# Kernel tuning notes

Measured on AMD Instinct MI355X. Metric: run time of the kernel, lower is better.

## Reference

```python
import jax, jax.numpy as jnp
import numpy as np
from jax import lax

N, D, K = 131072, 128, 1024
BETA = 1.0
EMA_DECAY = 0.85

def setup_inputs() -> dict:
    key = jax.random.key(0)
    k1, k2, k3, k4 = jax.random.split(key, 4)
    return {
        "x": jax.random.normal(k1, (N, D), dtype=jnp.float32),
        "embeddings": jax.random.uniform(k2, (D, K), dtype=jnp.float32),
        "ema_count": jax.random.uniform(k3, (K,), dtype=jnp.float32),
        "embeddings_sum": jax.random.uniform(k4, (D, K), dtype=jnp.float32),
    }

def reference(x, embeddings, ema_count, embeddings_sum):
    input_shape = x.shape
    flat = x.reshape(-1, D)                      # [N, D]
    # squared-euclidean distances via expanded ||a-b||^2
    sim = flat @ embeddings                      # [N, K]
    dist = (jnp.sum(flat ** 2, axis=1, keepdims=True)
            + jnp.sum(embeddings ** 2, axis=0)
            - 2.0 * sim)                         # [N, K]
    idx = jnp.argmin(dist, axis=1)               # [N] int
    # codebook lookup (gather instead of one-hot matmul)
    quantized = jnp.take(embeddings.T, idx, axis=0).reshape(input_shape)
    # EMA update (segment_sum instead of one-hot matmul scatter)
    count = jax.ops.segment_sum(jnp.ones((flat.shape[0],), flat.dtype), idx,
                                num_segments=K)                  # [K]
    ema_count_new = (1.0 - EMA_DECAY) * ema_count + EMA_DECAY * count
    sums = jax.ops.segment_sum(flat, idx, num_segments=K).T      # [D, K]
    embeddings_sum_new = (1.0 - EMA_DECAY) * embeddings_sum + EMA_DECAY * sums
    embeddings_new = embeddings_sum_new / jnp.maximum(ema_count_new, 1e-5)
    # losses (commitment added via add_loss in original)
    commitment_loss = jnp.mean((lax.stop_gradient(quantized) - x) ** 2)
    # straight-through estimator
    q_st = x + lax.stop_gradient(quantized - x)
    return q_st, embeddings_new, ema_count_new, embeddings_sum_new, BETA * commitment_loss
```

## Files before the change

kernel.cpp:

```cpp
#include <hip/hip_runtime.h>
#include <cfloat>
#include <cstdint>

#define NROWS 131072
#define DIMD  128
#define KCODE 1024
#define MARGIN 0.045f
#define RCAP  65536

typedef __attribute__((ext_vector_type(8))) _Float16 half8;
typedef __attribute__((ext_vector_type(4))) float f32x4;

union U4H8 { uint4 u; half8 h; };

#define WS_REFINE_CNT 0
#define WS_LOSS       8
#define WS_COUNTS     16
#define WS_SUMS       4608
#define WS_LPART      528896
#define WS_CURSOR     532992
#define WS_E2         537088
#define WS_ZERO_BYTES 541184
#define WS_ET         541184
#define WS_BHI        1065472
#define WS_BEST       1327616
#define WS_IDX        1589760
#define WS_ROWLIST    2114048
#define WS_REFINE     2638336
#define WS_PARTIALS   3162624

#define OUT_QST  ((size_t)0)
#define OUT_EMB  ((size_t)NROWS * DIMD)
#define OUT_CNT  (OUT_EMB + (size_t)DIMD * KCODE)
#define OUT_ES   (OUT_CNT + KCODE)
#define OUT_LOSS (OUT_ES + (size_t)DIMD * KCODE)

__device__ __forceinline__ unsigned f16pair(float a, float b) {
    union { _Float16 h[2]; unsigned u; } p;
    p.h[0] = (_Float16)a;
    p.h[1] = (_Float16)b;
    return p.u;
}

__global__ void vq_prep(const float* __restrict__ E, uint4* __restrict__ Bh,
                        float* __restrict__ ET, float* __restrict__ e2) {
    int gid = blockIdx.x * 256 + threadIdx.x;
    int l = gid & 63;
    int t = (gid >> 6) & 3;
    int NB = gid >> 8;
    int n = NB * 16 + (l & 15);
    int k0 = t * 32 + (l >> 4) * 8;
    float v[8];
    float ss = 0.f;
    #pragma unroll
    for (int j = 0; j < 8; ++j) {
        v[j] = E[(size_t)(k0 + j) * KCODE + n];
        ss = fmaf(v[j], v[j], ss);
    }
    Bh[gid] = make_uint4(f16pair(v[0], v[1]), f16pair(v[2], v[3]),
                         f16pair(v[4], v[5]), f16pair(v[6], v[7]));
    float4* et4 = (float4*)(ET + (size_t)n * DIMD + k0);
    et4[0] = make_float4(v[0], v[1], v[2], v[3]);
    et4[1] = make_float4(v[4], v[5], v[6], v[7]);
    atomicAdd(&e2[n], ss);
}


#define LOADB(bARR, ev_, nb_)                                     \
  { _Pragma("unroll")                                             \
    for (int t_ = 0; t_ < 4; ++t_)                                \
      bARR[t_] = Bh[((nb_) * 4 + t_) * 64 + l];                   \
    ev_ = e2[(nb_) * 16 + m]; }

#define COMPUTE_NB(nb_, bARR, ev_)                                           \
  {                                                                          \
    f32x4 acc[2];                                                            \
    _Pragma("unroll")                                                        \
    for (int mt_ = 0; mt_ < 2; ++mt_) acc[mt_] = (f32x4){0.f,0.f,0.f,0.f};   \
    _Pragma("unroll")                                                        \
    for (int t_ = 0; t_ < 4; ++t_) {                                         \
      U4H8 bh_; bh_.u = bARR[t_];                                            \
      _Pragma("unroll")                                                      \
      for (int mt_ = 0; mt_ < 2; ++mt_)                                      \
        acc[mt_] = __builtin_amdgcn_mfma_f32_16x16x32_f16(ah[mt_][t_], bh_.h,\
                                                          acc[mt_], 0, 0, 0);\
    }                                                                        \
    int col_ = (nb_) * 16 + m;                                               \
    _Pragma("unroll")                                                        \
    for (int mt_ = 0; mt_ < 2; ++mt_)                                        \
      _Pragma("unroll")                                                      \
      for (int r_ = 0; r_ < 4; ++r_) {                                       \
        float s_ = fmaf(-2.0f, acc[mt_][r_], ev_);                           \
        if (s_ < m1[mt_][r_]) {                                              \
          m2[mt_][r_] = m1[mt_][r_]; i2[mt_][r_] = i1[mt_][r_];              \
          m1[mt_][r_] = s_;          i1[mt_][r_] = col_;                     \
        } else if (s_ < m2[mt_][r_]) {                                       \
          m2[mt_][r_] = s_;          i2[mt_][r_] = col_;                     \
        }                                                                    \
      }                                                                      \
  }

__global__ __launch_bounds__(256, 2) void vq_argmin_mfma(
        const float* __restrict__ x, const uint4* __restrict__ Bh,
        const float* __restrict__ e2,
        int* __restrict__ idx, int* __restrict__ counts,
        int* __restrict__ refine_pairs, int* __restrict__ refine_cnt) {

    __shared__ int hist[KCODE];

    const int tid = threadIdx.x;
    const int w = tid >> 6, l = tid & 63;
    const int m = l & 15, q = l >> 4;
    const int rw = blockIdx.x * 128 + w * 32;

    uint4 bA[4], bB[4];
    float evA, evB;
    LOADB(bA, evA, 0);
    LOADB(bB, evB, 1);

    const float4* x4 = (const float4*)x;
    half8 ah[2][4];
    #pragma unroll
    for (int mt = 0; mt < 2; ++mt) {
        int row = rw + mt * 16 + m;
        #pragma unroll
        for (int t = 0; t < 4; ++t) {
            int c4 = t * 8 + q * 2;
            float4 va = x4[(size_t)row * 32 + c4];
            float4 vb = x4[(size_t)row * 32 + c4 + 1];
            half8 hh;
            hh[0] = (_Float16)va.x; hh[1] = (_Float16)va.y;
            hh[2] = (_Float16)va.z; hh[3] = (_Float16)va.w;
            hh[4] = (_Float16)vb.x; hh[5] = (_Float16)vb.y;
            hh[6] = (_Float16)vb.z; hh[7] = (_Float16)vb.w;
            ah[mt][t] = hh;
        }
    }

    float m1[2][4], m2[2][4];
    int i1[2][4], i2[2][4];
    #pragma unroll
    for (int a = 0; a < 2; ++a)
        #pragma unroll
        for (int r = 0; r < 4; ++r) {
            m1[a][r] = FLT_MAX; m2[a][r] = FLT_MAX;
            i1[a][r] = 0; i2[a][r] = 0;
        }

    for (int nb = 0; nb < 64; nb += 2) {
        COMPUTE_NB(nb, bA, evA);
        { int p = (nb + 2 <= 63) ? nb + 2 : 62; LOADB(bA, evA, p); }
        COMPUTE_NB(nb + 1, bB, evB);
        { int p = (nb + 3 <= 63) ? nb + 3 : 63; LOADB(bB, evB, p); }
    }

    #pragma unroll
    for (int mt = 0; mt < 2; ++mt)
        #pragma unroll
        for (int r = 0; r < 4; ++r) {
            float a1 = m1[mt][r], a2 = m2[mt][r];
            int ai1 = i1[mt][r], ai2 = i2[mt][r];
            #pragma unroll
            for (int off = 1; off < 16; off <<= 1) {
                float o1 = __shfl_xor(a1, off, 64);
                float o2 = __shfl_xor(a2, off, 64);
                int oi1 = __shfl_xor(ai1, off, 64);
                int oi2 = __shfl_xor(ai2, off, 64);
                bool take = (o1 < a1) || (o1 == a1 && oi1 < ai1);
                float w1 = take ? o1 : a1;  int wi1 = take ? oi1 : ai1;
                float l1 = take ? a1 : o1;  int li1 = take ? ai1 : oi1;
                float c2 = a2; int ci2 = ai2;
                if (o2 < c2 || (o2 == c2 && oi2 < ci2)) { c2 = o2; ci2 = oi2; }
                if (l1 < c2 || (l1 == c2 && li1 < ci2)) { c2 = l1; ci2 = li1; }
                a1 = w1; ai1 = wi1; a2 = c2; ai2 = ci2;
            }
            m1[mt][r] = a1; m2[mt][r] = a2;
            i1[mt][r] = ai1; i2[mt][r] = ai2;
        }

    for (int i = tid; i < KCODE; i += 256) hist[i] = 0;
    __syncthreads();
    if (m == 0) {
        #pragma unroll
        for (int mt = 0; mt < 2; ++mt)
            #pragma unroll
            for (int r = 0; r < 4; ++r) {
                int row = rw + mt * 16 + q * 4 + r;
                int bi = i1[mt][r];
                idx[row] = bi;
                atomicAdd(&hist[bi], 1);
                if (!(m2[mt][r] - m1[mt][r] > MARGIN)) {
                    int pos = atomicAdd(refine_cnt, 1);
                    if (pos < RCAP) {
                        refine_pairs[2 * pos]     = row;
                        refine_pairs[2 * pos + 1] = i2[mt][r];
                    }
                }
            }
    }
    __syncthreads();
    for (int i = tid; i < KCODE; i += 256) {
        int h = hist[i];
        if (h) atomicAdd(&counts[i], h);
    }
}

__global__ __launch_bounds__(256) void vq_refine2(
        const float* __restrict__ x, const float* __restrict__ ET,
        const float* __restrict__ e2,
        const int* __restrict__ refine_pairs, const int* __restrict__ refine_cnt,
        int* __restrict__ idx, int* __restrict__ counts) {
    int cnt = *refine_cnt;
    if (cnt > RCAP) cnt = RCAP;
    for (int e = blockIdx.x * 256 + threadIdx.x; e < cnt; e += gridDim.x * 256) {
        int n  = refine_pairs[2 * e];
        int kb = refine_pairs[2 * e + 1];
        int ka = idx[n];
        const float4* xa = (const float4*)(x + (size_t)n * DIMD);
        const float4* ea = (const float4*)(ET + (size_t)ka * DIMD);
        const float4* eb = (const float4*)(ET + (size_t)kb * DIMD);
        float da = 0.f, db = 0.f;
        #pragma unroll 8
        for (int d4 = 0; d4 < DIMD / 4; ++d4) {
            float4 xv = xa[d4];
            float4 av = ea[d4];
            float4 bv = eb[d4];
            da = fmaf(xv.x, av.x, da); da = fmaf(xv.y, av.y, da);
            da = fmaf(xv.z, av.z, da); da = fmaf(xv.w, av.w, da);
            db = fmaf(xv.x, bv.x, db); db = fmaf(xv.y, bv.y, db);
            db = fmaf(xv.z, bv.z, db); db = fmaf(xv.w, bv.w, db);
        }
        float sa = fmaf(-2.0f, da, e2[ka]);
        float sb = fmaf(-2.0f, db, e2[kb]);
        bool swap = (sb < sa) || (sb == sa && kb < ka);
        if (swap) {
            idx[n] = kb;
            atomicSub(&counts[ka], 1);
            atomicAdd(&counts[kb], 1);
        }
    }
}

__global__ void vq_scan(const int* __restrict__ counts, int* __restrict__ cursor) {
    __shared__ int s[KCODE];
    int t = threadIdx.x;
    int c = counts[t];
    s[t] = c;
    __syncthreads();
    for (int off = 1; off < KCODE; off <<= 1) {
        int v = (t >= off) ? s[t - off] : 0;
        __syncthreads();
        s[t] += v;
        __syncthreads();
    }
    cursor[t] = s[t] - c;
}

__global__ void vq_fill(const int* __restrict__ idx, int* __restrict__ cursor,
                        int* __restrict__ rowlist) {
    __shared__ int hcnt[KCODE];
    __shared__ int hbase[KCODE];
    int tid = threadIdx.x;
    for (int i = tid; i < KCODE; i += 256) hcnt[i] = 0;
    __syncthreads();
    int n = blockIdx.x * 256 + tid;
    int k = idx[n];
    int lrank = atomicAdd(&hcnt[k], 1);
    __syncthreads();
    for (int i = tid; i < KCODE; i += 256) {
        int h = hcnt[i];
        if (h) hbase[i] = atomicAdd(&cursor[i], h);
    }
    __syncthreads();
    rowlist[hbase[k] + lrank] = n;
}

__global__ void vq_chunksum(const float* __restrict__ x,
                            const int* __restrict__ rowlist,
                            const int* __restrict__ idx,
                            float* __restrict__ sums) {
    __shared__ int rl[128];
    __shared__ int kk[128];
    int tid = threadIdx.x;
    int base = blockIdx.x * 128;
    int r = rowlist[base + tid];
    rl[tid] = r;
    kk[tid] = idx[r];
    __syncthreads();
    float s = 0.f;
    int kprev = kk[0];
    #pragma unroll 4
    for (int j = 0; j < 128; ++j) {
        int kj = kk[j];
        if (kj != kprev) {
            atomicAdd(&sums[(size_t)kprev * DIMD + tid], s);
            s = 0.f;
            kprev = kj;
        }
        s += x[(size_t)rl[j] * DIMD + tid];
    }
    atomicAdd(&sums[(size_t)kprev * DIMD + tid], s);
}

__global__ void vq_quantize_loss(const float* __restrict__ x,
                                 const float* __restrict__ ET,
                                 const int* __restrict__ idx,
                                 float* __restrict__ out,
                                 float* __restrict__ lpart) {
    size_t gid = (size_t)blockIdx.x * 256 + threadIdx.x;
    size_t base = gid * 4;
    int n = (int)(base >> 7);
    int d = (int)(base & 127);
    int k = idx[n];
    float4 xv = *(const float4*)(x + base);
    float4 qv = *(const float4*)(ET + (size_t)k * DIMD + d);
    float t0 = qv.x - xv.x, t1 = qv.y - xv.y, t2 = qv.z - xv.z, t3 = qv.w - xv.w;
    float4 o;
    o.x = xv.x + t0; o.y = xv.y + t1; o.z = xv.z + t2; o.w = xv.w + t3;
    *(float4*)(out + OUT_QST + base) = o;
    float partial = t0 * t0 + t1 * t1 + t2 * t2 + t3 * t3;
    #pragma unroll
    for (int off = 32; off > 0; off >>= 1)
        partial += __shfl_down(partial, off);
    __shared__ float wsum[4];
    int wave = threadIdx.x >> 6;
    if ((threadIdx.x & 63) == 0) wsum[wave] = partial;
    __syncthreads();
    if (threadIdx.x == 0)
        atomicAdd(&lpart[blockIdx.x & 255], wsum[0] + wsum[1] + wsum[2] + wsum[3]);
}

__global__ void vq_finalize_emb(const int* __restrict__ counts,
                                const float* __restrict__ sums,
                                const float* __restrict__ emc,
                                const float* __restrict__ es,
                                const float* __restrict__ lpart,
                                float* __restrict__ out) {
    int gid = blockIdx.x * 256 + threadIdx.x;
    int k = gid & (KCODE - 1), d = gid >> 10;
    float cnt = (float)counts[k];
    float ecn = fmaf(0.85f, cnt, 0.15f * emc[k]);
    float esn = fmaf(0.85f, sums[(size_t)k * DIMD + d], 0.15f * es[(size_t)d * KCODE + k]);
    out[OUT_ES + (size_t)d * KCODE + k] = esn;
    out[OUT_EMB + (size_t)d * KCODE + k] = esn / fmaxf(ecn, 1e-5f);
    if (d == 0) out[OUT_CNT + k] = ecn;
    if (blockIdx.x == 0) {
        float v = lpart[threadIdx.x];
        #pragma unroll
        for (int off = 32; off > 0; off >>= 1)
            v += __shfl_down(v, off);
        __shared__ float ws4[4];
        if ((threadIdx.x & 63) == 0) ws4[threadIdx.x >> 6] = v;
        __syncthreads();
        if (threadIdx.x == 0)
            out[OUT_LOSS] = (ws4[0] + ws4[1] + ws4[2] + ws4[3]) /
                            ((float)NROWS * (float)DIMD);
    }
}

extern "C" void kernel_launch(void* const* d_in, const int* in_sizes, int n_in,
                              void* d_out, int out_size, void* d_ws, size_t ws_size,
                              hipStream_t stream) {
    const float* x   = (const float*)d_in[0];
    const float* E   = (const float*)d_in[1];
    const float* emc = (const float*)d_in[2];
    const float* es  = (const float*)d_in[3];
    float* out = (float*)d_out;
    char* ws = (char*)d_ws;

    int*    refine_cnt  = (int*)(ws + WS_REFINE_CNT);
    int*    counts      = (int*)(ws + WS_COUNTS);
    float*  sums        = (float*)(ws + WS_SUMS);
    float*  lpart       = (float*)(ws + WS_LPART);
    int*    cursor      = (int*)(ws + WS_CURSOR);
    float*  e2          = (float*)(ws + WS_E2);
    float*  ET          = (float*)(ws + WS_ET);
    uint4*  Bh          = (uint4*)(ws + WS_BHI);
    int*    idx         = (int*)(ws + WS_IDX);
    int*    rowlist     = (int*)(ws + WS_ROWLIST);
    int*    refine_pairs= (int*)(ws + WS_REFINE);

    hipMemsetAsync(ws, 0, WS_ZERO_BYTES, stream);

    vq_prep<<<64, 256, 0, stream>>>(E, Bh, ET, e2);
    vq_argmin_mfma<<<NROWS / 128, 256, 0, stream>>>(x, Bh, e2, idx, counts,
                                                    refine_pairs, refine_cnt);
    vq_refine2<<<256, 256, 0, stream>>>(x, ET, e2, refine_pairs, refine_cnt,
                                        idx, counts);
    vq_scan<<<1, KCODE, 0, stream>>>(counts, cursor);
    vq_fill<<<NROWS / 256, 256, 0, stream>>>(idx, cursor, rowlist);
    vq_chunksum<<<NROWS / 128, 128, 0, stream>>>(x, rowlist, idx, sums);
    vq_quantize_loss<<<(NROWS * (size_t)DIMD) / (256 * 4), 256, 0, stream>>>(x, ET, idx, out, lpart);
    vq_finalize_emb<<<(DIMD * KCODE) / 256, 256, 0, stream>>>(counts, sums, emc, es, lpart, out);
}
```

Measured before the change: 305.1 us.

## Halve argmin rows per wave and fuse quantize/loss into chunksum

The argmin kernel now gives each wave 16 rows instead of 32. That halves the A-fragment and top-2 register state, and launch bounds rise from 2 to 6 blocks for more occupancy, at the cost of reloading the codebook fragments twice as often per row. Separately, the quantize and commitment-loss kernel is removed. Its work is folded into the segment-sum kernel, which already reads each x row grouped by code, so one full pass over x and one launch are saved. The straight-through output is now written in row-scattered order per column thread and not as coalesced float4, which may hurt write efficiency.

```diff
diff --git a/kernel.cpp b/kernel.cpp
--- a/kernel.cpp
+++ b/kernel.cpp
@@ -74,33 +74,27 @@
 
 #define COMPUTE_NB(nb_, bARR, ev_)                                           \
   {                                                                          \
-    f32x4 acc[2];                                                            \
-    _Pragma("unroll")                                                        \
-    for (int mt_ = 0; mt_ < 2; ++mt_) acc[mt_] = (f32x4){0.f,0.f,0.f,0.f};   \
+    f32x4 acc = (f32x4){0.f, 0.f, 0.f, 0.f};                                 \
     _Pragma("unroll")                                                        \
     for (int t_ = 0; t_ < 4; ++t_) {                                         \
       U4H8 bh_; bh_.u = bARR[t_];                                            \
-      _Pragma("unroll")                                                      \
-      for (int mt_ = 0; mt_ < 2; ++mt_)                                      \
-        acc[mt_] = __builtin_amdgcn_mfma_f32_16x16x32_f16(ah[mt_][t_], bh_.h,\
-                                                          acc[mt_], 0, 0, 0);\
+      acc = __builtin_amdgcn_mfma_f32_16x16x32_f16(ah[t_], bh_.h,            \
+                                                   acc, 0, 0, 0);            \
     }                                                                        \
     int col_ = (nb_) * 16 + m;                                               \
     _Pragma("unroll")                                                        \
-    for (int mt_ = 0; mt_ < 2; ++mt_)                                        \
-      _Pragma("unroll")                                                      \
-      for (int r_ = 0; r_ < 4; ++r_) {                                       \
-        float s_ = fmaf(-2.0f, acc[mt_][r_], ev_);                           \
-        if (s_ < m1[mt_][r_]) {                                              \
-          m2[mt_][r_] = m1[mt_][r_]; i2[mt_][r_] = i1[mt_][r_];              \
-          m1[mt_][r_] = s_;          i1[mt_][r_] = col_;                     \
-        } else if (s_ < m2[mt_][r_]) {                                       \
-          m2[mt_][r_] = s_;          i2[mt_][r_] = col_;                     \
-        }                                                                    \
+    for (int r_ = 0; r_ < 4; ++r_) {                                         \
+      float s_ = fmaf(-2.0f, acc[r_], ev_);                                  \
+      if (s_ < m1[r_]) {                                                     \
+        m2[r_] = m1[r_]; i2[r_] = i1[r_];                                    \
+        m1[r_] = s_;     i1[r_] = col_;                                      \
+      } else if (s_ < m2[r_]) {                                              \
+        m2[r_] = s_;     i2[r_] = col_;                                      \
       }                                                                      \
+    }                                                                        \
   }
 
-__global__ __launch_bounds__(256, 2) void vq_argmin_mfma(
+__global__ __launch_bounds__(256, 6) void vq_argmin_mfma(
         const float* __restrict__ x, const uint4* __restrict__ Bh,
         const float* __restrict__ e2,
         int* __restrict__ idx, int* __restrict__ counts,
@@ -111,7 +105,7 @@
     const int tid = threadIdx.x;
     const int w = tid >> 6, l = tid & 63;
     const int m = l & 15, q = l >> 4;
-    const int rw = blockIdx.x * 128 + w * 32;
+    const int rw = blockIdx.x * 64 + w * 16;
 
     uint4 bA[4], bB[4];
     float evA, evB;
@@ -119,10 +113,9 @@
     LOADB(bB, evB, 1);
 
     const float4* x4 = (const float4*)x;
-    half8 ah[2][4];
-    #pragma unroll
-    for (int mt = 0; mt < 2; ++mt) {
-        int row = rw + mt * 16 + m;
+    half8 ah[4];
+    {
+        int row = rw + m;
         #pragma unroll
         for (int t = 0; t < 4; ++t) {
             int c4 = t * 8 + q * 2;
@@ -133,19 +126,17 @@
             hh[2] = (_Float16)va.z; hh[3] = (_Float16)va.w;
             hh[4] = (_Float16)vb.x; hh[5] = (_Float16)vb.y;
             hh[6] = (_Float16)vb.z; hh[7] = (_Float16)vb.w;
-            ah[mt][t] = hh;
-        }
-    }
-
-    float m1[2][4], m2[2][4];
-    int i1[2][4], i2[2][4];
+            ah[t] = hh;
+        }
+    }
+
+    float m1[4], m2[4];
+    int i1[4], i2[4];
     #pragma unroll
-    for (int a = 0; a < 2; ++a)
-        #pragma unroll
-        for (int r = 0; r < 4; ++r) {
-            m1[a][r] = FLT_MAX; m2[a][r] = FLT_MAX;
-            i1[a][r] = 0; i2[a][r] = 0;
-        }
+    for (int r = 0; r < 4; ++r) {
+        m1[r] = FLT_MAX; m2[r] = FLT_MAX;
+        i1[r] = 0; i2[r] = 0;
+    }
 
     for (int nb = 0; nb < 64; nb += 2) {
         COMPUTE_NB(nb, bA, evA);
@@ -155,48 +146,44 @@
     }
 
     #pragma unroll
-    for (int mt = 0; mt < 2; ++mt)
+    for (int r = 0; r < 4; ++r) {
+        float a1 = m1[r], a2 = m2[r];
+        int ai1 = i1[r], ai2 = i2[r];
+        #pragma unroll
+        for (int off = 1; off < 16; off <<= 1) {
+            float o1 = __shfl_xor(a1, off, 64);
+            float o2 = __shfl_xor(a2, off, 64);
+            int oi1 = __shfl_xor(ai1, off, 64);
+            int oi2 = __shfl_xor(ai2, off, 64);
+            bool take = (o1 < a1) || (o1 == a1 && oi1 < ai1);
+            float w1 = take ? o1 : a1;  int wi1 = take ? oi1 : ai1;
+            float l1 = take ? a1 : o1;  int li1 = take ? ai1 : oi1;
+            float c2 = a2; int ci2 = ai2;
+            if (o2 < c2 || (o2 == c2 && oi2 < ci2)) { c2 = o2; ci2 = oi2; }
+            if (l1 < c2 || (l1 == c2 && li1 < ci2)) { c2 = l1; ci2 = li1; }
+            a1 = w1; ai1 = wi1; a2 = c2; ai2 = ci2;
+        }
+        m1[r] = a1; m2[r] = a2;
+        i1[r] = ai1; i2[r] = ai2;
+    }
+
+    for (int i = tid; i < KCODE; i += 256) hist[i] = 0;
+    __syncthreads();
+    if (m == 0) {
         #pragma unroll
         for (int r = 0; r < 4; ++r) {
-            float a1 = m1[mt][r], a2 = m2[mt][r];
-            int ai1 = i1[mt][r], ai2 = i2[mt][r];
-            #pragma unroll
-            for (int off = 1; off < 16; off <<= 1) {
-                float o1 = __shfl_xor(a1, off, 64);
-                float o2 = __shfl_xor(a2, off, 64);
-                int oi1 = __shfl_xor(ai1, off, 64);
-                int oi2 = __shfl_xor(ai2, off, 64);
-                bool take = (o1 < a1) || (o1 == a1 && oi1 < ai1);
-                float w1 = take ? o1 : a1;  int wi1 = take ? oi1 : ai1;
-                float l1 = take ? a1 : o1;  int li1 = take ? ai1 : oi1;
-                float c2 = a2; int ci2 = ai2;
-                if (o2 < c2 || (o2 == c2 && oi2 < ci2)) { c2 = o2; ci2 = oi2; }
-                if (l1 < c2 || (l1 == c2 && li1 < ci2)) { c2 = l1; ci2 = li1; }
-                a1 = w1; ai1 = wi1; a2 = c2; ai2 = ci2;
-            }
-            m1[mt][r] = a1; m2[mt][r] = a2;
-            i1[mt][r] = ai1; i2[mt][r] = ai2;
-        }
-
-    for (int i = tid; i < KCODE; i += 256) hist[i] = 0;
-    __syncthreads();
-    if (m == 0) {
-        #pragma unroll
-        for (int mt = 0; mt < 2; ++mt)
-            #pragma unroll
-            for (int r = 0; r < 4; ++r) {
-                int row = rw + mt * 16 + q * 4 + r;
-                int bi = i1[mt][r];
-                idx[row] = bi;
-                atomicAdd(&hist[bi], 1);
-                if (!(m2[mt][r] - m1[mt][r] > MARGIN)) {
-                    int pos = atomicAdd(refine_cnt, 1);
-                    if (pos < RCAP) {
-                        refine_pairs[2 * pos]     = row;
-                        refine_pairs[2 * pos + 1] = i2[mt][r];
-                    }
+            int row = rw + q * 4 + r;
+            int bi = i1[r];
+            idx[row] = bi;
+            atomicAdd(&hist[bi], 1);
+            if (!(m2[r] - m1[r] > MARGIN)) {
+                int pos = atomicAdd(refine_cnt, 1);
+                if (pos < RCAP) {
+                    refine_pairs[2 * pos]     = row;
+                    refine_pairs[2 * pos + 1] = i2[r];
                 }
             }
+        }
     }
     __syncthreads();
     for (int i = tid; i < KCODE; i += 256) {
@@ -278,17 +265,22 @@
 __global__ void vq_chunksum(const float* __restrict__ x,
                             const int* __restrict__ rowlist,
                             const int* __restrict__ idx,
-                            float* __restrict__ sums) {
+                            const float* __restrict__ ET,
+                            float* __restrict__ sums,
+                            float* __restrict__ out,
+                            float* __restrict__ lpart) {
     __shared__ int rl[128];
     __shared__ int kk[128];
+    __shared__ float wsum[2];
     int tid = threadIdx.x;
     int base = blockIdx.x * 128;
     int r = rowlist[base + tid];
     rl[tid] = r;
     kk[tid] = idx[r];
     __syncthreads();
-    float s = 0.f;
+    float s = 0.f, lossp = 0.f;
     int kprev = kk[0];
+    float qreg = ET[(size_t)kprev * DIMD + tid];
     #pragma unroll 4
     for (int j = 0; j < 128; ++j) {
         int kj = kk[j];
@@ -296,38 +288,23 @@
             atomicAdd(&sums[(size_t)kprev * DIMD + tid], s);
             s = 0.f;
             kprev = kj;
-        }
-        s += x[(size_t)rl[j] * DIMD + tid];
+            qreg = ET[(size_t)kj * DIMD + tid];
+        }
+        size_t off = (size_t)rl[j] * DIMD + tid;
+        float xv = x[off];
+        s += xv;
+        float diff = qreg - xv;
+        out[OUT_QST + off] = xv + diff;
+        lossp = fmaf(diff, diff, lossp);
     }
     atomicAdd(&sums[(size_t)kprev * DIMD + tid], s);
-}
-
-__global__ void vq_quantize_loss(const float* __restrict__ x,
-                                 const float* __restrict__ ET,
-                                 const int* __restrict__ idx,
-                                 float* __restrict__ out,
-                                 float* __restrict__ lpart) {
-    size_t gid = (size_t)blockIdx.x * 256 + threadIdx.x;
-    size_t base = gid * 4;
-    int n = (int)(base >> 7);
-    int d = (int)(base & 127);
-    int k = idx[n];
-    float4 xv = *(const float4*)(x + base);
-    float4 qv = *(const float4*)(ET + (size_t)k * DIMD + d);
-    float t0 = qv.x - xv.x, t1 = qv.y - xv.y, t2 = qv.z - xv.z, t3 = qv.w - xv.w;
-    float4 o;
-    o.x = xv.x + t0; o.y = xv.y + t1; o.z = xv.z + t2; o.w = xv.w + t3;
-    *(float4*)(out + OUT_QST + base) = o;
-    float partial = t0 * t0 + t1 * t1 + t2 * t2 + t3 * t3;
     #pragma unroll
     for (int off = 32; off > 0; off >>= 1)
-        partial += __shfl_down(partial, off);
-    __shared__ float wsum[4];
-    int wave = threadIdx.x >> 6;
-    if ((threadIdx.x & 63) == 0) wsum[wave] = partial;
-    __syncthreads();
-    if (threadIdx.x == 0)
-        atomicAdd(&lpart[blockIdx.x & 255], wsum[0] + wsum[1] + wsum[2] + wsum[3]);
+        lossp += __shfl_down(lossp, off);
+    if ((tid & 63) == 0) wsum[tid >> 6] = lossp;
+    __syncthreads();
+    if (tid == 0)
+        atomicAdd(&lpart[blockIdx.x & 255], wsum[0] + wsum[1]);
 }
 
 __global__ void vq_finalize_emb(const int* __restrict__ counts,
@@ -383,13 +360,13 @@
     hipMemsetAsync(ws, 0, WS_ZERO_BYTES, stream);
 
     vq_prep<<<64, 256, 0, stream>>>(E, Bh, ET, e2);
-    vq_argmin_mfma<<<NROWS / 128, 256, 0, stream>>>(x, Bh, e2, idx, counts,
-                                                    refine_pairs, refine_cnt);
+    vq_argmin_mfma<<<NROWS / 64, 256, 0, stream>>>(x, Bh, e2, idx, counts,
+                                                   refine_pairs, refine_cnt);
     vq_refine2<<<256, 256, 0, stream>>>(x, ET, e2, refine_pairs, refine_cnt,
                                         idx, counts);
     vq_scan<<<1, KCODE, 0, stream>>>(counts, cursor);
     vq_fill<<<NROWS / 256, 256, 0, stream>>>(idx, cursor, rowlist);
-    vq_chunksum<<<NROWS / 128, 128, 0, stream>>>(x, rowlist, idx, sums);
-    vq_quantize_loss<<<(NROWS * (size_t)DIMD) / (256 * 4), 256, 0, stream>>>(x, ET, idx, out, lpart);
+    vq_chunksum<<<NROWS / 128, 128, 0, stream>>>(x, rowlist, idx, ET, sums,
+                                                 out, lpart);
     vq_finalize_emb<<<(DIMD * KCODE) / 256, 256, 0, stream>>>(counts, sums, emc, es, lpart, out);
 }
```

Result: slower. 316.2 us (+3.6%).
